# Optimization experiments

Hardware: AMD Instinct MI355X
Metric: run time of the kernel (lower is better)

The kernel has to match this reference:

```python
import jax, jax.numpy as jnp
import numpy as np

B, T, C = 1, 4096, 2048
NH, HS, NQG = 16, 128, 4          # n_head, head_size, n_query_groups (GQA)
Q_PER_KV = NH // NQG              # 4
QKV_DIM = (NH + 2 * NQG) * HS     # 3072
ROT = HS // 2                     # rotary half-dim = 64


def setup_inputs() -> dict:
    key = jax.random.key(0)
    k0, k1, k2 = jax.random.split(key, 3)
    x = jax.random.normal(k0, (B, T, C), dtype=jnp.float32)
    W_attn = jax.random.normal(k1, (QKV_DIM, C), dtype=jnp.float32) * 0.02
    W_proj = jax.random.normal(k2, (C, C), dtype=jnp.float32) * 0.02
    # RoPE cache: cos/sin of shape (T, head_size/2), flash-attn convention
    inv_freq = 1.0 / (10000.0 ** (jnp.arange(0, HS, 2, dtype=jnp.float32) / HS))
    freqs = jnp.arange(T, dtype=jnp.float32)[:, None] * inv_freq[None, :]
    return {"x": x, "cos": jnp.cos(freqs), "sin": jnp.sin(freqs),
            "W_attn": W_attn, "W_proj": W_proj}


def _apply_rope(t, cos, sin):
    # t: (B, T, H, HS); cos/sin: (T, ROT). Non-interleaved (rotate-half) form.
    x1, x2 = t[..., :ROT], t[..., ROT:]
    c = cos[None, :, None, :]
    s = sin[None, :, None, :]
    return jnp.concatenate([x1 * c - x2 * s, x2 * c + x1 * s], axis=-1)


def reference(x, cos, sin, W_attn, W_proj):
    Bx, Tx, Cx = x.shape
    qkv = jnp.einsum('btc,fc->btf', x, W_attn)                 # (B,T,3072)
    qkv = qkv.reshape(Bx, Tx, NQG, Q_PER_KV + 2, HS)
    q = qkv[:, :, :, :Q_PER_KV, :].reshape(Bx, Tx, NH, HS)     # (B,T,16,128)
    k = qkv[:, :, :, Q_PER_KV, :]                              # (B,T,4,128)
    v = qkv[:, :, :, Q_PER_KV + 1, :]                          # (B,T,4,128)
    q = _apply_rope(q, cos, sin)
    k = _apply_rope(k, cos, sin)
    # GQA: expand kv groups to match query heads (repeat_interleave on head dim)
    k = jnp.repeat(k, Q_PER_KV, axis=2)                        # (B,T,16,128)
    v = jnp.repeat(v, Q_PER_KV, axis=2)
    scale = 1.0 / np.sqrt(HS).astype(np.float32)
    scores = jnp.einsum('bthd,bshd->bhts', q, k) * scale       # (B,H,T,T)
    causal = jnp.tril(jnp.ones((Tx, Tx), dtype=bool))
    scores = jnp.where(causal[None, None], scores, jnp.finfo(scores.dtype).min)
    attn = jax.nn.softmax(scores, axis=-1)
    y = jnp.einsum('bhts,bshd->bthd', attn, v).reshape(Bx, Tx, Cx)
    return jnp.einsum('btc,oc->bto', y, W_proj)
```

## Files before the change

### kernel.cpp

```cpp
#include <hip/hip_runtime.h>
#include <hip/hip_bf16.h>

typedef __hip_bfloat16 bf16;
typedef __attribute__((ext_vector_type(8))) short short8;
typedef __attribute__((ext_vector_type(4))) short short4v;
typedef __attribute__((ext_vector_type(4))) float floatx4;

#define T_SEQ 4096
#define C_DIM 2048
#define NHEAD 16
#define HSZ   128
#define NGRP  4

#define MFMA_BF16(A,B,C) __builtin_amdgcn_mfma_f32_16x16x32_bf16((A),(B),(C),0,0,0)

__device__ __forceinline__ void gld_lds16(const bf16* g, bf16* l) {
  __builtin_amdgcn_global_load_lds(
      (__attribute__((address_space(1))) void*)(g),
      (__attribute__((address_space(3))) void*)(l), 16, 0, 0);
}

__global__ void cvt_kernel(const float* __restrict__ src, bf16* __restrict__ dst, long n)
{
  const long i = ((long)blockIdx.x * blockDim.x + threadIdx.x) * 8;
  if (i >= n) return;
  const float4 a = *(const float4*)(src + i);
  const float4 b = *(const float4*)(src + i + 4);
  bf16 tmp[8];
  tmp[0] = __float2bfloat16(a.x); tmp[1] = __float2bfloat16(a.y);
  tmp[2] = __float2bfloat16(a.z); tmp[3] = __float2bfloat16(a.w);
  tmp[4] = __float2bfloat16(b.x); tmp[5] = __float2bfloat16(b.y);
  tmp[6] = __float2bfloat16(b.z); tmp[7] = __float2bfloat16(b.w);
  *(short8*)(dst + i) = *(const short8*)tmp;
}

__global__ __launch_bounds__(256, 3)
void gemm_bt_kernel(const bf16* __restrict__ A, const bf16* __restrict__ B,
                    float* __restrict__ Cf, bf16* __restrict__ Cq,
                    bf16* __restrict__ Ck, bf16* __restrict__ Cvt,
                    int K, int qkv_mode)
{
  __shared__ alignas(16) bf16 As[128 * 64];
  __shared__ alignas(16) bf16 Bs[128 * 64];

  const int t  = threadIdx.x;
  const int w  = t >> 6, l = t & 63;
  const int wr = w >> 1, wc = w & 1;
  const int q4 = l >> 4, ln = l & 15;
  const long bm = (long)blockIdx.y * 128;
  const long bn = (long)blockIdx.x * 128;

  floatx4 acc[4][4] = {};

  const bf16* Ab = A + (bm + t / 8) * (long)K + (t % 8) * 8;
  const bf16* Bb = B + (bn + t / 8) * (long)K + (t % 8) * 8;

  for (int k0 = 0; k0 < K; k0 += 64) {
    __syncthreads();
#pragma unroll
    for (int i = 0; i < 4; ++i) {
      gld_lds16(Ab + (long)i * 32 * K + k0, As + (i * 256 + w * 64) * 8);
      gld_lds16(Bb + (long)i * 32 * K + k0, Bs + (i * 256 + w * 64) * 8);
    }
    __syncthreads();
#pragma unroll
    for (int kk = 0; kk < 64; kk += 32) {
      short8 af[4], bfr[4];
      const int co = kk + q4 * 8;
#pragma unroll
      for (int mi = 0; mi < 4; ++mi)
        af[mi] = *(const short8*)(As + (wr * 64 + mi * 16 + ln) * 64 + co);
#pragma unroll
      for (int ni = 0; ni < 4; ++ni)
        bfr[ni] = *(const short8*)(Bs + (wc * 64 + ni * 16 + ln) * 64 + co);
#pragma unroll
      for (int mi = 0; mi < 4; ++mi)
#pragma unroll
        for (int ni = 0; ni < 4; ++ni)
          acc[mi][ni] = MFMA_BF16(af[mi], bfr[ni], acc[mi][ni]);
    }
  }

  if (!qkv_mode) {
#pragma unroll
    for (int mi = 0; mi < 4; ++mi) {
      const long r0 = bm + wr * 64 + mi * 16 + q4 * 4;
#pragma unroll
      for (int ni = 0; ni < 4; ++ni) {
        const long c = bn + wc * 64 + ni * 16 + ln;
#pragma unroll
        for (int r = 0; r < 4; ++r)
          Cf[(r0 + r) * C_DIM + c] = acc[mi][ni][r];
      }
    }
  } else {
    const int cb = blockIdx.x;
    const int g = cb / 6, slot = cb - g * 6;
    if (slot == 5) {
      bf16* dstv = Cvt + (long)g * HSZ * T_SEQ;
#pragma unroll
      for (int pass = 0; pass < 2; ++pass) {
        __syncthreads();
        if (wc == pass) {
#pragma unroll
          for (int mi = 0; mi < 4; ++mi) {
            const int tc = wr * 64 + mi * 16 + q4 * 4;
#pragma unroll
            for (int ni = 0; ni < 4; ++ni) {
              const int dr = ni * 16 + ln;
              short4v pk;
#pragma unroll
              for (int r = 0; r < 4; ++r) {
                bf16 v = __float2bfloat16(acc[mi][ni][r]);
                pk[r] = *(short*)&v;
              }
              *(short4v*)(As + dr * 128 + tc) = pk;
            }
          }
        }
        __syncthreads();
        const int row = t >> 2, ch = (t & 3) * 32;
        bf16* gp = dstv + (long)(pass * 64 + row) * T_SEQ + bm + ch;
#pragma unroll
        for (int jj = 0; jj < 4; ++jj)
          *(short8*)(gp + jj * 8) = *(const short8*)(As + row * 128 + ch + jj * 8);
      }
    } else {
      bf16* dst = (slot < 4) ? (Cq + (long)(g * 4 + slot) * T_SEQ * HSZ)
                             : (Ck + (long)g * T_SEQ * HSZ);
#pragma unroll
      for (int mi = 0; mi < 4; ++mi) {
        const long r0 = bm + wr * 64 + mi * 16 + q4 * 4;
#pragma unroll
        for (int ni = 0; ni < 4; ++ni) {
          const long c = wc * 64 + ni * 16 + ln;
#pragma unroll
          for (int r = 0; r < 4; ++r)
            dst[(r0 + r) * HSZ + c] = __float2bfloat16(acc[mi][ni][r]);
        }
      }
    }
  }
}

__global__ void rope_kernel(bf16* __restrict__ Q, bf16* __restrict__ Kb,
                            const float* __restrict__ cs, const float* __restrict__ sn)
{
  const long idx = (long)blockIdx.x * blockDim.x + threadIdx.x;
  const long NQ = (long)NHEAD * T_SEQ * 8;
  bf16* buf; long rem; float qs;
  if (idx < NQ) { buf = Q;  rem = idx;      qs = 0.08838834764831845f * 1.4426950408889634f; }
  else          { buf = Kb; rem = idx - NQ; qs = 1.0f; }
  const int d0 = (int)(rem & 7) * 8;
  const int tt = (int)((rem >> 3) & (T_SEQ - 1));
  const int hh = (int)(rem >> 15);
  const float4 c0 = *(const float4*)(cs + tt * 64 + d0);
  const float4 c1 = *(const float4*)(cs + tt * 64 + d0 + 4);
  const float4 s0 = *(const float4*)(sn + tt * 64 + d0);
  const float4 s1 = *(const float4*)(sn + tt * 64 + d0 + 4);
  float cc[8] = {c0.x,c0.y,c0.z,c0.w,c1.x,c1.y,c1.z,c1.w};
  float ss[8] = {s0.x,s0.y,s0.z,s0.w,s1.x,s1.y,s1.z,s1.w};
  bf16* p = buf + ((long)hh * T_SEQ + tt) * HSZ + d0;
  short8 v1 = *(const short8*)(p);
  short8 v2 = *(const short8*)(p + 64);
  short8 o1, o2;
#pragma unroll
  for (int jj = 0; jj < 8; ++jj) {
    short u1 = v1[jj], u2 = v2[jj];
    const float x1 = __bfloat162float(*(bf16*)&u1);
    const float x2 = __bfloat162float(*(bf16*)&u2);
    bf16 y1 = __float2bfloat16((x1 * cc[jj] - x2 * ss[jj]) * qs);
    bf16 y2 = __float2bfloat16((x2 * cc[jj] + x1 * ss[jj]) * qs);
    o1[jj] = *(short*)&y1; o2[jj] = *(short*)&y2;
  }
  *(short8*)(p)      = o1;
  *(short8*)(p + 64) = o2;
}

__global__ __launch_bounds__(256, 2)
void attn_kernel(const bf16* __restrict__ Qg, const bf16* __restrict__ Kg,
                 const bf16* __restrict__ Vtg, bf16* __restrict__ Y,
                 bf16* __restrict__ Opart, float* __restrict__ Lpart)
{
  __shared__ alignas(16) bf16 Ks[64][132];
  __shared__ alignas(16) bf16 Vt[128][68];
  __shared__ alignas(16) bf16 Ps[128][68];

  const int id   = blockIdx.x;
  const int h    = id / 48;
  const int r48  = id - h * 48;
  const int c    = r48 / 3, slot = r48 - c * 3;
  const int P    = (slot == 0) ? c : (31 - c);
  const int j0   = (slot == 2) ? (32 - c) : 0;
  const int j1   = (slot == 0) ? (2 * c + 2) : ((slot == 1) ? (32 - c) : (64 - 2 * c));
  const int g    = h >> 2;

  const int t = threadIdx.x;
  const int w = t >> 6, l = t & 63;
  const int q4 = l >> 4, ln = l & 15;

  const bf16* Qh = Qg + (long)h * T_SEQ * HSZ;
  const bf16* Kh = Kg + (long)g * T_SEQ * HSZ;
  const bf16* Vh = Vtg + (long)g * HSZ * T_SEQ;

  const int qbase = P * 128 + w * 32;

  short8 qf[2][4];
#pragma unroll
  for (int mi = 0; mi < 2; ++mi) {
    const long row = qbase + mi * 16 + ln;
#pragma unroll
    for (int ks = 0; ks < 4; ++ks)
      qf[mi][ks] = *(const short8*)(Qh + row * HSZ + ks * 32 + q4 * 8);
  }

  short8 ones_f;
#pragma unroll
  for (int i = 0; i < 8; ++i) ones_f[i] = (ln == 0) ? (short)0x3F80 : (short)0;

  floatx4 acc[2][8] = {};
  floatx4 acc_l[2] = {};

  const int krow = t >> 4, kc = (t & 15) * 8;
  const int vrow = t >> 3, vc = (t & 7) * 8;

  short8 kpre[4], vpre[4];
  {
    const int sb = j0 * 64;
#pragma unroll
    for (int i = 0; i < 4; ++i) {
      kpre[i] = *(const short8*)(Kh + (long)(sb + krow + 16 * i) * HSZ + kc);
      vpre[i] = *(const short8*)(Vh + (long)(vrow + 32 * i) * T_SEQ + sb + vc);
    }
  }

  for (int j = j0; j < j1; ++j) {
    const int s0 = j * 64;
#pragma unroll
    for (int i = 0; i < 4; ++i) {
      *(short8*)(&Ks[krow + 16 * i][kc]) = kpre[i];
      *(short8*)(&Vt[vrow + 32 * i][vc]) = vpre[i];
    }
    __syncthreads();
    if (j + 1 < j1) {
      const int s1 = s0 + 64;
#pragma unroll
      for (int i = 0; i < 4; ++i) {
        kpre[i] = *(const short8*)(Kh + (long)(s1 + krow + 16 * i) * HSZ + kc);
        vpre[i] = *(const short8*)(Vh + (long)(vrow + 32 * i) * T_SEQ + s1 + vc);
      }
    }

    floatx4 sacc[2][4] = {};
#pragma unroll
    for (int ks = 0; ks < 4; ++ks) {
      short8 kf[4];
#pragma unroll
      for (int ni = 0; ni < 4; ++ni)
        kf[ni] = *(const short8*)(&Ks[ni * 16 + ln][ks * 32 + q4 * 8]);
#pragma unroll
      for (int mi = 0; mi < 2; ++mi)
#pragma unroll
        for (int ni = 0; ni < 4; ++ni)
          sacc[mi][ni] = MFMA_BF16(qf[mi][ks], kf[ni], sacc[mi][ni]);
    }

#pragma unroll
    for (int mi = 0; mi < 2; ++mi) {
      const int base_m = qbase + mi * 16 + q4 * 4 - s0 - ln;
#pragma unroll
      for (int ni = 0; ni < 4; ++ni)
#pragma unroll
        for (int r = 0; r < 4; ++r) {
          float pv = __builtin_amdgcn_exp2f(sacc[mi][ni][r]);
          if (base_m + r - ni * 16 < 0) pv = 0.f;
          Ps[w * 32 + mi * 16 + q4 * 4 + r][ni * 16 + ln] = __float2bfloat16(pv);
        }
    }

#pragma unroll
    for (int ks = 0; ks < 2; ++ks) {
      short8 pf[2], vf[8];
#pragma unroll
      for (int mi = 0; mi < 2; ++mi)
        pf[mi] = *(const short8*)(&Ps[w * 32 + mi * 16 + ln][ks * 32 + q4 * 8]);
#pragma unroll
      for (int nd = 0; nd < 8; ++nd)
        vf[nd] = *(const short8*)(&Vt[nd * 16 + ln][ks * 32 + q4 * 8]);
#pragma unroll
      for (int mi = 0; mi < 2; ++mi) {
        acc_l[mi] = MFMA_BF16(pf[mi], ones_f, acc_l[mi]);
#pragma unroll
        for (int nd = 0; nd < 8; ++nd)
          acc[mi][nd] = MFMA_BF16(pf[mi], vf[nd], acc[mi][nd]);
      }
    }
    __syncthreads();
  }

  if (slot == 0) {
#pragma unroll
    for (int mi = 0; mi < 2; ++mi) {
#pragma unroll
      for (int r = 0; r < 4; ++r) {
        const float lv = __shfl(acc_l[mi][r], l & 48, 64);
        const float inv = (lv > 0.f) ? 1.f / lv : 0.f;
        const long tq = qbase + mi * 16 + q4 * 4 + r;
#pragma unroll
        for (int nd = 0; nd < 8; ++nd)
          Y[tq * C_DIM + h * HSZ + nd * 16 + ln] = __float2bfloat16(acc[mi][nd][r] * inv);
      }
    }
  } else {
    const int sidx = (h * 16 + (P - 16)) * 2 + (slot - 1);
    bf16* Op = Opart + (long)sidx * (128 * 128);
    float* Lp = Lpart + sidx * 128;
#pragma unroll
    for (int mi = 0; mi < 2; ++mi) {
#pragma unroll
      for (int r = 0; r < 4; ++r) {
        const int row = w * 32 + mi * 16 + q4 * 4 + r;
        if (ln == 0) Lp[row] = acc_l[mi][r];
#pragma unroll
        for (int nd = 0; nd < 8; ++nd)
          Op[row * 128 + nd * 16 + ln] = __float2bfloat16(acc[mi][nd][r]);
      }
    }
  }
}

__global__ void combine_kernel(const bf16* __restrict__ Opart,
                               const float* __restrict__ Lpart,
                               bf16* __restrict__ Y)
{
  const int b = blockIdx.x;
  const int h = b >> 4, pp = b & 15;
  const bf16* O0 = Opart + (long)b * 2 * 16384;
  const bf16* O1 = O0 + 16384;
  const float* L0 = Lpart + b * 256;
  const float* L1 = L0 + 128;
  const long qb = (long)(pp + 16) * 128;
  const int t = threadIdx.x;
#pragma unroll
  for (int it = 0; it < 8; ++it) {
    const int idx = it * 2048 + t * 8;
    const int row = idx >> 7, d = idx & 127;
    const float lsum = L0[row] + L1[row];
    const float inv = (lsum > 0.f) ? 1.f / lsum : 0.f;
    const short8 a = *(const short8*)(O0 + idx);
    const short8 bb = *(const short8*)(O1 + idx);
    short8 o;
#pragma unroll
    for (int jj = 0; jj < 8; ++jj) {
      short ua = a[jj], ub = bb[jj];
      const float fa = __bfloat162float(*(bf16*)&ua);
      const float fb = __bfloat162float(*(bf16*)&ub);
      bf16 y = __float2bfloat16((fa + fb) * inv);
      o[jj] = *(short*)&y;
    }
    *(short8*)(Y + (qb + row) * C_DIM + h * HSZ + d) = o;
  }
}

extern "C" void kernel_launch(void* const* d_in, const int* in_sizes, int n_in,
                              void* d_out, int out_size, void* d_ws, size_t ws_size,
                              hipStream_t stream)
{
  const float* x  = (const float*)d_in[0];
  const float* cs = (const float*)d_in[1];
  const float* sn = (const float*)d_in[2];
  const float* Wa = (const float*)d_in[3];
  const float* Wp = (const float*)d_in[4];
  float* out = (float*)d_out;

  const long nx  = (long)T_SEQ * C_DIM;
  const long nwa = (long)(NHEAD + 2 * NGRP) * HSZ * C_DIM;
  const long nwp = (long)C_DIM * C_DIM;
  const long nqh = (long)NHEAD * T_SEQ * HSZ;
  const long nkg = (long)NGRP * T_SEQ * HSZ;

  const size_t need = (size_t)(nx + nwa + nqh + 2 * nkg + nqh) * sizeof(bf16);
  if (ws_size < need) return;

  bf16* xb  = (bf16*)d_ws;
  bf16* Wab = xb + nx;
  bf16* Q   = Wab + nwa;
  bf16* K   = Q + nqh;
  bf16* Vt  = K + nkg;
  bf16* Y   = Vt + nkg;
  bf16* Wpb = Q;
  bf16* Opart = xb;
  float* Lpart = (float*)Wab;

  cvt_kernel<<<(int)(nx  / 8 / 256), 256, 0, stream>>>(x,  xb,  nx);
  cvt_kernel<<<(int)(nwa / 8 / 256), 256, 0, stream>>>(Wa, Wab, nwa);
  gemm_bt_kernel<<<dim3(24, 32), 256, 0, stream>>>(xb, Wab, nullptr, Q, K, Vt, C_DIM, 1);
  rope_kernel<<<2560, 256, 0, stream>>>(Q, K, cs, sn);
  attn_kernel<<<768, 256, 0, stream>>>(Q, K, Vt, Y, Opart, Lpart);
  combine_kernel<<<256, 256, 0, stream>>>(Opart, Lpart, Y);
  cvt_kernel<<<(int)(nwp / 8 / 256), 256, 0, stream>>>(Wp, Wpb, nwp);
  gemm_bt_kernel<<<dim3(16, 32), 256, 0, stream>>>(Y, Wpb, out, nullptr, nullptr, nullptr, C_DIM, 0);
}
```

Measured before the change: 372.1 us.

## Rebalance causal attention work into 512 equal-cost blocks with two phases

Replaces the 768-block three-slot causal work split with 512 blocks. Each 'A' block handles a short diagonal query tile and then the tail part of a long tile. Each 'B' block handles the first 33 KV tiles of a long tile. This is meant to balance per-block work at 33 KV tiles and reduce launch and tail imbalance; the partial results for the long tiles still go through the combine kernel. In exchange, A blocks run two sequential phases that reload Q and reinitialize accumulators.

Result: faster. 335.6 us (-9.8%).

```diff
diff --git a/kernel.cpp b/kernel.cpp
--- a/kernel.cpp
+++ b/kernel.cpp
@@ -186,14 +186,12 @@
   __shared__ alignas(16) bf16 Vt[128][68];
   __shared__ alignas(16) bf16 Ps[128][68];
 
-  const int id   = blockIdx.x;
-  const int h    = id / 48;
-  const int r48  = id - h * 48;
-  const int c    = r48 / 3, slot = r48 - c * 3;
-  const int P    = (slot == 0) ? c : (31 - c);
-  const int j0   = (slot == 2) ? (32 - c) : 0;
-  const int j1   = (slot == 0) ? (2 * c + 2) : ((slot == 1) ? (32 - c) : (64 - 2 * c));
-  const int g    = h >> 2;
+  const int id  = blockIdx.x;
+  const int h   = id >> 5;
+  const int r   = id & 31;
+  const int c   = r >> 1;
+  const int isA = r & 1;
+  const int g   = h >> 2;
 
   const int t = threadIdx.x;
   const int w = t >> 6, l = t & 63;
@@ -203,127 +201,134 @@
   const bf16* Kh = Kg + (long)g * T_SEQ * HSZ;
   const bf16* Vh = Vtg + (long)g * HSZ * T_SEQ;
 
-  const int qbase = P * 128 + w * 32;
-
-  short8 qf[2][4];
-#pragma unroll
-  for (int mi = 0; mi < 2; ++mi) {
-    const long row = qbase + mi * 16 + ln;
-#pragma unroll
-    for (int ks = 0; ks < 4; ++ks)
-      qf[mi][ks] = *(const short8*)(Qh + row * HSZ + ks * 32 + q4 * 8);
-  }
-
   short8 ones_f;
 #pragma unroll
   for (int i = 0; i < 8; ++i) ones_f[i] = (ln == 0) ? (short)0x3F80 : (short)0;
-
-  floatx4 acc[2][8] = {};
-  floatx4 acc_l[2] = {};
 
   const int krow = t >> 4, kc = (t & 15) * 8;
   const int vrow = t >> 3, vc = (t & 7) * 8;
 
-  short8 kpre[4], vpre[4];
-  {
-    const int sb = j0 * 64;
-#pragma unroll
-    for (int i = 0; i < 4; ++i) {
-      kpre[i] = *(const short8*)(Kh + (long)(sb + krow + 16 * i) * HSZ + kc);
-      vpre[i] = *(const short8*)(Vh + (long)(vrow + 32 * i) * T_SEQ + sb + vc);
-    }
-  }
-
-  for (int j = j0; j < j1; ++j) {
-    const int s0 = j * 64;
-#pragma unroll
-    for (int i = 0; i < 4; ++i) {
-      *(short8*)(&Ks[krow + 16 * i][kc]) = kpre[i];
-      *(short8*)(&Vt[vrow + 32 * i][vc]) = vpre[i];
-    }
-    __syncthreads();
-    if (j + 1 < j1) {
-      const int s1 = s0 + 64;
+  const int nph = isA ? 2 : 1;
+  for (int ph = 0; ph < nph; ++ph) {
+    const int P      = (isA && ph == 0) ? c : (31 - c);
+    const int jlo    = (isA && ph == 1) ? 33 : 0;
+    const int jhi    = isA ? (ph == 0 ? (2 * c + 2) : (64 - 2 * c)) : 33;
+    const bool direct = (isA && ph == 0);
+    const int qbase  = P * 128 + w * 32;
+
+    short8 qf[2][4];
+#pragma unroll
+    for (int mi = 0; mi < 2; ++mi) {
+      const long row = qbase + mi * 16 + ln;
+#pragma unroll
+      for (int ks = 0; ks < 4; ++ks)
+        qf[mi][ks] = *(const short8*)(Qh + row * HSZ + ks * 32 + q4 * 8);
+    }
+
+    floatx4 acc[2][8] = {};
+    floatx4 acc_l[2] = {};
+
+    short8 kpre[4], vpre[4];
+    {
+      const int sb = jlo * 64;
 #pragma unroll
       for (int i = 0; i < 4; ++i) {
-        kpre[i] = *(const short8*)(Kh + (long)(s1 + krow + 16 * i) * HSZ + kc);
-        vpre[i] = *(const short8*)(Vh + (long)(vrow + 32 * i) * T_SEQ + s1 + vc);
-      }
-    }
-
-    floatx4 sacc[2][4] = {};
-#pragma unroll
-    for (int ks = 0; ks < 4; ++ks) {
-      short8 kf[4];
-#pragma unroll
-      for (int ni = 0; ni < 4; ++ni)
-        kf[ni] = *(const short8*)(&Ks[ni * 16 + ln][ks * 32 + q4 * 8]);
-#pragma unroll
-      for (int mi = 0; mi < 2; ++mi)
+        kpre[i] = *(const short8*)(Kh + (long)(sb + krow + 16 * i) * HSZ + kc);
+        vpre[i] = *(const short8*)(Vh + (long)(vrow + 32 * i) * T_SEQ + sb + vc);
+      }
+    }
+
+    for (int j = jlo; j < jhi; ++j) {
+      const int s0 = j * 64;
+#pragma unroll
+      for (int i = 0; i < 4; ++i) {
+        *(short8*)(&Ks[krow + 16 * i][kc]) = kpre[i];
+        *(short8*)(&Vt[vrow + 32 * i][vc]) = vpre[i];
+      }
+      __syncthreads();
+      if (j + 1 < jhi) {
+        const int s1 = s0 + 64;
+#pragma unroll
+        for (int i = 0; i < 4; ++i) {
+          kpre[i] = *(const short8*)(Kh + (long)(s1 + krow + 16 * i) * HSZ + kc);
+          vpre[i] = *(const short8*)(Vh + (long)(vrow + 32 * i) * T_SEQ + s1 + vc);
+        }
+      }
+
+      floatx4 sacc[2][4] = {};
+#pragma unroll
+      for (int ks = 0; ks < 4; ++ks) {
+        short8 kf[4];
 #pragma unroll
         for (int ni = 0; ni < 4; ++ni)
-          sacc[mi][ni] = MFMA_BF16(qf[mi][ks], kf[ni], sacc[mi][ni]);
-    }
-
-#pragma unroll
-    for (int mi = 0; mi < 2; ++mi) {
-      const int base_m = qbase + mi * 16 + q4 * 4 - s0 - ln;
-#pragma unroll
-      for (int ni = 0; ni < 4; ++ni)
-#pragma unroll
-        for (int r = 0; r < 4; ++r) {
-          float pv = __builtin_amdgcn_exp2f(sacc[mi][ni][r]);
-          if (base_m + r - ni * 16 < 0) pv = 0.f;
-          Ps[w * 32 + mi * 16 + q4 * 4 + r][ni * 16 + ln] = __float2bfloat16(pv);
-        }
-    }
-
-#pragma unroll
-    for (int ks = 0; ks < 2; ++ks) {
-      short8 pf[2], vf[8];
-#pragma unroll
-      for (int mi = 0; mi < 2; ++mi)
-        pf[mi] = *(const short8*)(&Ps[w * 32 + mi * 16 + ln][ks * 32 + q4 * 8]);
-#pragma unroll
-      for (int nd = 0; nd < 8; ++nd)
-        vf[nd] = *(const short8*)(&Vt[nd * 16 + ln][ks * 32 + q4 * 8]);
+          kf[ni] = *(const short8*)(&Ks[ni * 16 + ln][ks * 32 + q4 * 8]);
+#pragma unroll
+        for (int mi = 0; mi < 2; ++mi)
+#pragma unroll
+          for (int ni = 0; ni < 4; ++ni)
+            sacc[mi][ni] = MFMA_BF16(qf[mi][ks], kf[ni], sacc[mi][ni]);
+      }
+
 #pragma unroll
       for (int mi = 0; mi < 2; ++mi) {
-        acc_l[mi] = MFMA_BF16(pf[mi], ones_f, acc_l[mi]);
+        const int base_m = qbase + mi * 16 + q4 * 4 - s0 - ln;
+#pragma unroll
+        for (int ni = 0; ni < 4; ++ni)
+#pragma unroll
+          for (int r2 = 0; r2 < 4; ++r2) {
+            float pv = __builtin_amdgcn_exp2f(sacc[mi][ni][r2]);
+            if (base_m + r2 - ni * 16 < 0) pv = 0.f;
+            Ps[w * 32 + mi * 16 + q4 * 4 + r2][ni * 16 + ln] = __float2bfloat16(pv);
+          }
+      }
+
+#pragma unroll
+      for (int ks = 0; ks < 2; ++ks) {
+        short8 pf[2], vf[8];
+#pragma unroll
+        for (int mi = 0; mi < 2; ++mi)
+          pf[mi] = *(const short8*)(&Ps[w * 32 + mi * 16 + ln][ks * 32 + q4 * 8]);
 #pragma unroll
         for (int nd = 0; nd < 8; ++nd)
-          acc[mi][nd] = MFMA_BF16(pf[mi], vf[nd], acc[mi][nd]);
-      }
-    }
-    __syncthreads();
-  }
-
-  if (slot == 0) {
-#pragma unroll
-    for (int mi = 0; mi < 2; ++mi) {
-#pragma unroll
-      for (int r = 0; r < 4; ++r) {
-        const float lv = __shfl(acc_l[mi][r], l & 48, 64);
-        const float inv = (lv > 0.f) ? 1.f / lv : 0.f;
-        const long tq = qbase + mi * 16 + q4 * 4 + r;
-#pragma unroll
-        for (int nd = 0; nd < 8; ++nd)
-          Y[tq * C_DIM + h * HSZ + nd * 16 + ln] = __float2bfloat16(acc[mi][nd][r] * inv);
-      }
-    }
-  } else {
-    const int sidx = (h * 16 + (P - 16)) * 2 + (slot - 1);
-    bf16* Op = Opart + (long)sidx * (128 * 128);
-    float* Lp = Lpart + sidx * 128;
-#pragma unroll
-    for (int mi = 0; mi < 2; ++mi) {
-#pragma unroll
-      for (int r = 0; r < 4; ++r) {
-        const int row = w * 32 + mi * 16 + q4 * 4 + r;
-        if (ln == 0) Lp[row] = acc_l[mi][r];
-#pragma unroll
-        for (int nd = 0; nd < 8; ++nd)
-          Op[row * 128 + nd * 16 + ln] = __float2bfloat16(acc[mi][nd][r]);
+          vf[nd] = *(const short8*)(&Vt[nd * 16 + ln][ks * 32 + q4 * 8]);
+#pragma unroll
+        for (int mi = 0; mi < 2; ++mi) {
+          acc_l[mi] = MFMA_BF16(pf[mi], ones_f, acc_l[mi]);
+#pragma unroll
+          for (int nd = 0; nd < 8; ++nd)
+            acc[mi][nd] = MFMA_BF16(pf[mi], vf[nd], acc[mi][nd]);
+        }
+      }
+      __syncthreads();
+    }
+
+    if (direct) {
+#pragma unroll
+      for (int mi = 0; mi < 2; ++mi) {
+#pragma unroll
+        for (int r2 = 0; r2 < 4; ++r2) {
+          const float lv = __shfl(acc_l[mi][r2], l & 48, 64);
+          const float inv = (lv > 0.f) ? 1.f / lv : 0.f;
+          const long tq = qbase + mi * 16 + q4 * 4 + r2;
+#pragma unroll
+          for (int nd = 0; nd < 8; ++nd)
+            Y[tq * C_DIM + h * HSZ + nd * 16 + ln] = __float2bfloat16(acc[mi][nd][r2] * inv);
+        }
+      }
+    } else {
+      const int sidx = (h * 16 + (15 - c)) * 2 + isA;
+      bf16* Op = Opart + (long)sidx * (128 * 128);
+      float* Lp = Lpart + sidx * 128;
+#pragma unroll
+      for (int mi = 0; mi < 2; ++mi) {
+#pragma unroll
+        for (int r2 = 0; r2 < 4; ++r2) {
+          const int row = w * 32 + mi * 16 + q4 * 4 + r2;
+          if (ln == 0) Lp[row] = acc_l[mi][r2];
+#pragma unroll
+          for (int nd = 0; nd < 8; ++nd)
+            Op[row * 128 + nd * 16 + ln] = __float2bfloat16(acc[mi][nd][r2]);
+        }
       }
     }
   }
@@ -396,7 +401,7 @@
   cvt_kernel<<<(int)(nwa / 8 / 256), 256, 0, stream>>>(Wa, Wab, nwa);
   gemm_bt_kernel<<<dim3(24, 32), 256, 0, stream>>>(xb, Wab, nullptr, Q, K, Vt, C_DIM, 1);
   rope_kernel<<<2560, 256, 0, stream>>>(Q, K, cs, sn);
-  attn_kernel<<<768, 256, 0, stream>>>(Q, K, Vt, Y, Opart, Lpart);
+  attn_kernel<<<512, 256, 0, stream>>>(Q, K, Vt, Y, Opart, Lpart);
   combine_kernel<<<256, 256, 0, stream>>>(Opart, Lpart, Y);
   cvt_kernel<<<(int)(nwp / 8 / 256), 256, 0, stream>>>(Wp, Wpb, nwp);
   gemm_bt_kernel<<<dim3(16, 32), 256, 0, stream>>>(Y, Wpb, out, nullptr, nullptr, nullptr, C_DIM, 0);
```
